# Kernel tuning notes

Hardware: AMD Instinct MI355X
Metric: run time of the kernel (lower is better)

The kernel has to match this reference:

```python
import jax, jax.numpy as jnp
import numpy as np

N_NODES = 50000
N_EDGES = 800000
D_IN = 128
D_OUT = 128


def setup_inputs() -> dict:
    key = jax.random.key(0)
    k1, k2, k3, k4 = jax.random.split(key, 4)
    X = jax.random.normal(k1, (N_NODES, D_IN), dtype=jnp.float32)
    weight = jax.random.normal(k2, (D_IN, D_OUT), dtype=jnp.float32) * (1.0 / np.sqrt(D_OUT))
    edge_src = jax.random.randint(k3, (N_EDGES,), 0, N_NODES, dtype=jnp.int32)
    edge_dst = jax.random.randint(k4, (N_EDGES,), 0, N_NODES, dtype=jnp.int32)
    return {"X": X, "weight": weight, "edge_src": edge_src, "edge_dst": edge_dst}


def reference(X, weight, edge_src, edge_dst):
    # GCN: out = A_hat_hat @ (X @ W), A_hat_hat = D^-1/2 (A + I) D^-1/2
    ones = jnp.ones((edge_src.shape[0],), dtype=X.dtype)
    # node degrees (+1 for implicit self loop, avoids div-by-zero)
    deg = jax.ops.segment_sum(ones, edge_dst, num_segments=N_NODES) + 1.0
    inv_sqrt_deg = jax.lax.rsqrt(deg)  # [N]
    XW = X @ weight  # [N, D_OUT] dense GEMM
    # per-edge normalization 1/sqrt(d_i * d_j)
    norm = inv_sqrt_deg[edge_dst] * inv_sqrt_deg[edge_src]  # [E]
    msg = XW[edge_src] * norm[:, None]  # [E, D_OUT] gather
    agg = jax.ops.segment_sum(msg, edge_dst, num_segments=N_NODES)  # scatter-add
    # self-loop contribution: 1/d_i * XW[i]
    out = agg + XW * (inv_sqrt_deg * inv_sqrt_deg)[:, None]
    return out
```

## Files before the change

### kernel.cpp

```cpp
#include <hip/hip_runtime.h>

#define N_NODES 50000
#define N_EDGES 800000
#define D 128

#define NBLK 256
#define EPB (N_EDGES / NBLK)
#define NBKT 196
#define CAP 6144

typedef __attribute__((ext_vector_type(8))) short bf16x8;
typedef __attribute__((ext_vector_type(4))) float f32x4;

static const size_t OFF_TOT  = 0;
static const size_t OFF_WT   = 1024;
static const size_t OFF_H    = 33792;
static const size_t OFF_BB   = 234496;
static const size_t OFF_DEG  = 435200;
static const size_t OFF_OFFS = 635200;
static const size_t OFF_IVS  = 835200;
static const size_t OFF_REC  = 1235200;
static const size_t OFF_CSR  = 6052096;
static const size_t OFF_XWQ  = 8460544;

#define BM 64
#define NB_GEMM ((N_NODES + BM - 1) / BM)

__device__ __forceinline__ unsigned short f2bf(float f) {
    unsigned int u = __float_as_uint(f);
    unsigned int r = (u + 0x7fffu + ((u >> 16) & 1u)) >> 16;
    return (unsigned short)r;
}
__device__ __forceinline__ float sb(unsigned int u, int i) {
    return (float)((int)(u << (24 - 8 * i)) >> 24);
}

__global__ __launch_bounds__(256) void k_pre(const int* __restrict__ dst,
                                             int* __restrict__ H,
                                             const float* __restrict__ W,
                                             unsigned short* __restrict__ Wt) {
    __shared__ unsigned int cnt[256];
    int bid = blockIdx.x, t = threadIdx.x;
    if (bid >= NBLK) {
        int idx = (bid - NBLK) * 256 + t;
        int n = idx >> 7, k = idx & 127;
        Wt[n * D + k] = f2bf(W[k * D + n]);
        return;
    }
    cnt[t] = 0;
    __syncthreads();
    int e0 = bid * EPB;
    for (int i = t; i < EPB; i += 256)
        atomicAdd(&cnt[dst[e0 + i] >> 8], 1u);
    __syncthreads();
    if (t < NBKT) H[t * NBLK + bid] = (int)cnt[t];
}

__global__ __launch_bounds__(256) void k_pB(const int* __restrict__ H,
                                            int* __restrict__ BB,
                                            int* __restrict__ TOT) {
    int k = blockIdx.x, t = threadIdx.x;
    int w = t >> 6, l = t & 63;
    int v = H[k * NBLK + t];
    int s = v;
    #pragma unroll
    for (int d = 1; d < 64; d <<= 1) {
        int u = __shfl_up(s, d, 64);
        if (l >= d) s += u;
    }
    __shared__ int wtot[4], woff[4];
    if (l == 63) wtot[w] = s;
    __syncthreads();
    if (t == 0) {
        woff[0] = 0; woff[1] = wtot[0];
        woff[2] = wtot[0] + wtot[1]; woff[3] = wtot[0] + wtot[1] + wtot[2];
    }
    __syncthreads();
    int excl = s - v + woff[w];
    BB[k * NBLK + t] = excl;
    if (t == 255) TOT[k] = excl + v;
}

__global__ __launch_bounds__(512) void k_pC(const int* __restrict__ src,
                                            const int* __restrict__ dst,
                                            const int* __restrict__ BB,
                                            unsigned int* __restrict__ rec) {
    __shared__ unsigned int cnt[200];
    __shared__ int myBB[NBKT];
    int b = blockIdx.x, t = threadIdx.x;
    if (t < 200) cnt[t] = 0;
    if (t < NBKT) myBB[t] = t * CAP + BB[t * NBLK + b];
    __syncthreads();
    int e0 = b * EPB;
    for (int i = t; i < EPB; i += 512) {
        int e = e0 + i;
        int d = dst[e];
        int k = d >> 8;
        unsigned int r = atomicAdd(&cnt[k], 1u);
        rec[myBB[k] + (int)r] = (unsigned int)src[e] | ((unsigned int)(d & 255) << 16);
    }
}

__global__ __launch_bounds__(256) void k_mid(const unsigned int* __restrict__ rec,
                                             const int* __restrict__ TOT,
                                             int* __restrict__ deg,
                                             int* __restrict__ offs,
                                             float* __restrict__ ivs,
                                             unsigned short* __restrict__ csr,
                                             const float* __restrict__ X,
                                             const unsigned short* __restrict__ Wt,
                                             char* __restrict__ XWq) {
    __shared__ unsigned short sA[BM * D];
    __shared__ unsigned short sB[D * D];
    __shared__ int wtot[4], woff[4];
    int bid = blockIdx.x;
    int t = threadIdx.x;
    int w = t >> 6, l = t & 63;

    if (bid >= NBKT) {
        int r0 = (bid - NBKT) * BM;

        #pragma unroll
        for (int p = 0; p < 8; ++p) {
            int e = p * 2048 + t * 8;
            int n = e >> 7, k = e & 127;
            uint4 v = *(const uint4*)&Wt[e];
            int idx = n * D + (((k >> 3) ^ (n & 7)) << 3);
            *(uint4*)&sB[idx] = v;
        }
        #pragma unroll
        for (int p = 0; p < 8; ++p) {
            int e = p * 1024 + t * 4;
            int r = e >> 7, c = e & 127;
            int row = r0 + r;
            float4 xv = make_float4(0.f, 0.f, 0.f, 0.f);
            if (row < N_NODES) xv = *(const float4*)&X[row * D + c];
            ushort4 bv;
            bv.x = f2bf(xv.x); bv.y = f2bf(xv.y); bv.z = f2bf(xv.z); bv.w = f2bf(xv.w);
            int idx = r * D + (((c >> 3) ^ (r & 7)) << 3) + (c & 7);
            *(ushort4*)&sA[idx] = bv;
        }
        __syncthreads();

        int arow = w * 16 + (l & 15);
        f32x4 acc[8];
        #pragma unroll
        for (int i = 0; i < 8; ++i) acc[i] = (f32x4){0.f, 0.f, 0.f, 0.f};

        #pragma unroll
        for (int kk = 0; kk < 4; ++kk) {
            int g = kk * 4 + (l >> 4);
            bf16x8 a = *(bf16x8*)&sA[arow * D + ((g ^ (arow & 7)) << 3)];
            #pragma unroll
            for (int nt = 0; nt < 8; ++nt) {
                int nrow = nt * 16 + (l & 15);
                bf16x8 b = *(bf16x8*)&sB[nrow * D + ((g ^ (nrow & 7)) << 3)];
                acc[nt] = __builtin_amdgcn_mfma_f32_16x16x32_bf16(a, b, acc[nt], 0, 0, 0);
            }
        }

        float rmax[4];
        #pragma unroll
        for (int r = 0; r < 4; ++r) {
            float m = 0.f;
            #pragma unroll
            for (int nt = 0; nt < 8; ++nt) m = fmaxf(m, fabsf(acc[nt][r]));
            #pragma unroll
            for (int d = 1; d < 16; d <<= 1) m = fmaxf(m, __shfl_xor(m, d, 64));
            rmax[r] = fmaxf(m, 1e-20f);
        }

        __syncthreads();
        char* sQ = (char*)sA;
        #pragma unroll
        for (int r = 0; r < 4; ++r) {
            float qs = 127.0f / rmax[r];
            int row = w * 16 + (l >> 4) * 4 + r;
            #pragma unroll
            for (int nt = 0; nt < 8; ++nt) {
                float f = acc[nt][r] * qs;
                f = fminf(fmaxf(f, -127.0f), 127.0f);
                sQ[row * D + nt * 16 + (l & 15)] = (char)__float2int_rn(f);
            }
            if ((l & 15) == 0) {
                int m = r0 + row;
                if (m < N_NODES) ivs[m * 2 + 1] = rmax[r] * (1.0f / 127.0f);
            }
        }
        __syncthreads();

        int limit = (N_NODES - r0) * D;
        if (limit > BM * D) limit = BM * D;
        const uint4* q4 = (const uint4*)sQ;
        uint4* dst4 = (uint4*)(XWq + (size_t)r0 * D);
        if (t * 16 < limit) dst4[t] = q4[t];
        if ((t + 256) * 16 < limit) dst4[t + 256] = q4[t + 256];
        return;
    }

    unsigned int* lcnt = (unsigned int*)sA;
    int* off_l = ((int*)sA) + 256;
    int k = bid;
    int base = k * CAP;
    int tot = TOT[k];

    lcnt[t] = 0;
    __syncthreads();
    for (int i = t; i < tot; i += 256)
        atomicAdd(&lcnt[rec[base + i] >> 16], 1u);
    __syncthreads();

    int v = (int)lcnt[t];
    int s = v;
    #pragma unroll
    for (int d = 1; d < 64; d <<= 1) {
        int u = __shfl_up(s, d, 64);
        if (l >= d) s += u;
    }
    if (l == 63) wtot[w] = s;
    __syncthreads();
    if (t == 0) {
        woff[0] = 0; woff[1] = wtot[0];
        woff[2] = wtot[0] + wtot[1]; woff[3] = wtot[0] + wtot[1] + wtot[2];
    }
    __syncthreads();
    int excl = s - v + woff[w];
    off_l[t] = excl;
    int node = k * 256 + t;
    if (node < N_NODES) {
        deg[node] = v;
        ivs[node * 2] = rsqrtf((float)v + 1.0f);
        offs[node] = base + excl;
    }
    __syncthreads();
    lcnt[t] = 0;
    __syncthreads();
    for (int i = t; i < tot; i += 256) {
        unsigned int rc = rec[base + i];
        int dl = rc >> 16;
        unsigned int r = atomicAdd(&lcnt[dl], 1u);
        csr[base + off_l[dl] + (int)r] = (unsigned short)(rc & 0xFFFFu);
    }
}

__global__ __launch_bounds__(256) void k_agg(const char* __restrict__ XWq,
                                             const float2* __restrict__ ivs,
                                             const unsigned short* __restrict__ csr,
                                             const int* __restrict__ offs,
                                             const int* __restrict__ deg,
                                             float* __restrict__ out) {
    int node = blockIdx.x * 4 + (threadIdx.x >> 6);
    if (node >= N_NODES) return;
    int l = threadIdx.x & 63;
    int eg = l >> 4;
    int cl = l & 15;

    int start = offs[node];
    int cnt = deg[node];
    float2 vs0 = ivs[node];
    float invd = vs0.x;

    float acc[8];
    #pragma unroll
    for (int j = 0; j < 8; ++j) acc[j] = 0.f;

    if (eg == 0) {
        float sc = invd * invd * vs0.y;
        uint2 v = *(const uint2*)&XWq[(size_t)node * D + cl * 8];
        acc[0] += sc * sb(v.x, 0); acc[1] += sc * sb(v.x, 1);
        acc[2] += sc * sb(v.x, 2); acc[3] += sc * sb(v.x, 3);
        acc[4] += sc * sb(v.y, 0); acc[5] += sc * sb(v.y, 1);
        acc[6] += sc * sb(v.y, 2); acc[7] += sc * sb(v.y, 3);
    }

    for (int e = eg; e < cnt; e += 16) {
        int s[4];
        #pragma unroll
        for (int u = 0; u < 4; ++u) {
            int ee = e + u * 4;
            s[u] = (ee < cnt) ? (int)csr[start + ee] : -1;
        }
        uint2 v[4];
        float nn[4];
        #pragma unroll
        for (int u = 0; u < 4; ++u) {
            int si = (s[u] >= 0) ? s[u] : s[0];
            v[u] = *(const uint2*)&XWq[(size_t)si * D + cl * 8];
            float2 iv = ivs[si];
            nn[u] = (s[u] >= 0) ? invd * iv.x * iv.y : 0.f;
        }
        #pragma unroll
        for (int u = 0; u < 4; ++u) {
            float n = nn[u];
            acc[0] += n * sb(v[u].x, 0); acc[1] += n * sb(v[u].x, 1);
            acc[2] += n * sb(v[u].x, 2); acc[3] += n * sb(v[u].x, 3);
            acc[4] += n * sb(v[u].y, 0); acc[5] += n * sb(v[u].y, 1);
            acc[6] += n * sb(v[u].y, 2); acc[7] += n * sb(v[u].y, 3);
        }
    }

    #pragma unroll
    for (int j = 0; j < 8; ++j) {
        acc[j] += __shfl_xor(acc[j], 16, 64);
        acc[j] += __shfl_xor(acc[j], 32, 64);
    }

    if (l < 16) {
        float4 v0 = make_float4(acc[0], acc[1], acc[2], acc[3]);
        float4 v1 = make_float4(acc[4], acc[5], acc[6], acc[7]);
        *(float4*)&out[node * D + cl * 8] = v0;
        *(float4*)&out[node * D + cl * 8 + 4] = v1;
    }
}

extern "C" void kernel_launch(void* const* d_in, const int* in_sizes, int n_in,
                              void* d_out, int out_size, void* d_ws, size_t ws_size,
                              hipStream_t stream) {
    const float* X = (const float*)d_in[0];
    const float* W = (const float*)d_in[1];
    const int* esrc = (const int*)d_in[2];
    const int* edst = (const int*)d_in[3];
    float* out = (float*)d_out;

    char* ws = (char*)d_ws;
    int* TOT = (int*)(ws + OFF_TOT);
    unsigned short* Wt = (unsigned short*)(ws + OFF_WT);
    int* H = (int*)(ws + OFF_H);
    int* BB = (int*)(ws + OFF_BB);
    int* deg = (int*)(ws + OFF_DEG);
    int* offs = (int*)(ws + OFF_OFFS);
    float* ivs = (float*)(ws + OFF_IVS);
    unsigned int* rec = (unsigned int*)(ws + OFF_REC);
    unsigned short* csr = (unsigned short*)(ws + OFF_CSR);
    char* XWq = (char*)(ws + OFF_XWQ);

    k_pre<<<NBLK + 64, 256, 0, stream>>>(edst, H, W, Wt);
    k_pB<<<NBKT, 256, 0, stream>>>(H, BB, TOT);
    k_pC<<<NBLK, 512, 0, stream>>>(esrc, edst, BB, rec);
    k_mid<<<NBKT + NB_GEMM, 256, 0, stream>>>(rec, TOT, deg, offs, ivs, csr,
                                              X, Wt, XWq);
    k_agg<<<(N_NODES + 3) / 4, 256, 0, stream>>>(XWq, (const float2*)ivs, csr,
                                                 offs, deg, out);
}
```

Measured before the change: 63.68 us.

## Vectorize edge loads, pad CSR rows, and remap aggregation to 16 lanes per node

Block count for the edge-bucketing passes changes to 250 so each block's edge range is a multiple of four, which lets the histogram and scatter kernels read dst/src as int4. Per-node CSR segments are padded to a multiple of four with zero entries, so aggregation can fetch eight source indices per iteration with two 8-byte loads. The aggregation kernel now gives each node 16 lanes that walk all of its edges with eight gathers in flight, which removes the cross-lane shuffle reduction and packs 16 nodes per block. The trade-off is fewer parallel edge groups per node and reads of a few padded or neighbouring CSR entries whose contributions are masked out.

```diff
diff --git a/kernel.cpp b/kernel.cpp
--- a/kernel.cpp
+++ b/kernel.cpp
@@ -4,8 +4,9 @@
 #define N_EDGES 800000
 #define D 128
 
-#define NBLK 256
+#define NBLK 250
 #define EPB (N_EDGES / NBLK)
+#define NQ (EPB / 4)
 #define NBKT 196
 #define CAP 6144
 
@@ -50,10 +51,15 @@
     cnt[t] = 0;
     __syncthreads();
     int e0 = bid * EPB;
-    for (int i = t; i < EPB; i += 256)
-        atomicAdd(&cnt[dst[e0 + i] >> 8], 1u);
-    __syncthreads();
-    if (t < NBKT) H[t * NBLK + bid] = (int)cnt[t];
+    for (int q = t; q < NQ; q += 256) {
+        int4 d4 = *(const int4*)&dst[e0 + q * 4];
+        atomicAdd(&cnt[d4.x >> 8], 1u);
+        atomicAdd(&cnt[d4.y >> 8], 1u);
+        atomicAdd(&cnt[d4.z >> 8], 1u);
+        atomicAdd(&cnt[d4.w >> 8], 1u);
+    }
+    __syncthreads();
+    if (t < NBKT) H[t * 256 + bid] = (int)cnt[t];
 }
 
 __global__ __launch_bounds__(256) void k_pB(const int* __restrict__ H,
@@ -61,7 +67,7 @@
                                             int* __restrict__ TOT) {
     int k = blockIdx.x, t = threadIdx.x;
     int w = t >> 6, l = t & 63;
-    int v = H[k * NBLK + t];
+    int v = (t < NBLK) ? H[k * 256 + t] : 0;
     int s = v;
     #pragma unroll
     for (int d = 1; d < 64; d <<= 1) {
@@ -77,7 +83,7 @@
     }
     __syncthreads();
     int excl = s - v + woff[w];
-    BB[k * NBLK + t] = excl;
+    BB[k * 256 + t] = excl;
     if (t == 255) TOT[k] = excl + v;
 }
 
@@ -89,15 +95,32 @@
     __shared__ int myBB[NBKT];
     int b = blockIdx.x, t = threadIdx.x;
     if (t < 200) cnt[t] = 0;
-    if (t < NBKT) myBB[t] = t * CAP + BB[t * NBLK + b];
+    if (t < NBKT) myBB[t] = t * CAP + BB[t * 256 + b];
     __syncthreads();
     int e0 = b * EPB;
-    for (int i = t; i < EPB; i += 512) {
-        int e = e0 + i;
-        int d = dst[e];
-        int k = d >> 8;
-        unsigned int r = atomicAdd(&cnt[k], 1u);
-        rec[myBB[k] + (int)r] = (unsigned int)src[e] | ((unsigned int)(d & 255) << 16);
+    for (int q = t; q < NQ; q += 512) {
+        int4 d4 = *(const int4*)&dst[e0 + q * 4];
+        int4 s4 = *(const int4*)&src[e0 + q * 4];
+        {
+            int k = d4.x >> 8;
+            unsigned int r = atomicAdd(&cnt[k], 1u);
+            rec[myBB[k] + (int)r] = (unsigned int)s4.x | ((unsigned int)(d4.x & 255) << 16);
+        }
+        {
+            int k = d4.y >> 8;
+            unsigned int r = atomicAdd(&cnt[k], 1u);
+            rec[myBB[k] + (int)r] = (unsigned int)s4.y | ((unsigned int)(d4.y & 255) << 16);
+        }
+        {
+            int k = d4.z >> 8;
+            unsigned int r = atomicAdd(&cnt[k], 1u);
+            rec[myBB[k] + (int)r] = (unsigned int)s4.z | ((unsigned int)(d4.z & 255) << 16);
+        }
+        {
+            int k = d4.w >> 8;
+            unsigned int r = atomicAdd(&cnt[k], 1u);
+            rec[myBB[k] + (int)r] = (unsigned int)s4.w | ((unsigned int)(d4.w & 255) << 16);
+        }
     }
 }
 
@@ -211,7 +234,8 @@
     __syncthreads();
 
     int v = (int)lcnt[t];
-    int s = v;
+    int vr = (v + 3) & ~3;
+    int s = vr;
     #pragma unroll
     for (int d = 1; d < 64; d <<= 1) {
         int u = __shfl_up(s, d, 64);
@@ -224,7 +248,7 @@
         woff[2] = wtot[0] + wtot[1]; woff[3] = wtot[0] + wtot[1] + wtot[2];
     }
     __syncthreads();
-    int excl = s - v + woff[w];
+    int excl = s - vr + woff[w];
     off_l[t] = excl;
     int node = k * 256 + t;
     if (node < N_NODES) {
@@ -232,6 +256,7 @@
         ivs[node * 2] = rsqrtf((float)v + 1.0f);
         offs[node] = base + excl;
     }
+    for (int j = v; j < vr; ++j) csr[base + excl + j] = 0;
     __syncthreads();
     lcnt[t] = 0;
     __syncthreads();
@@ -249,48 +274,56 @@
                                              const int* __restrict__ offs,
                                              const int* __restrict__ deg,
                                              float* __restrict__ out) {
-    int node = blockIdx.x * 4 + (threadIdx.x >> 6);
-    if (node >= N_NODES) return;
-    int l = threadIdx.x & 63;
-    int eg = l >> 4;
-    int cl = l & 15;
-
-    int start = offs[node];
-    int cnt = deg[node];
-    float2 vs0 = ivs[node];
-    float invd = vs0.x;
+    __shared__ int s_off[16];
+    __shared__ int s_cnt[16];
+    __shared__ float2 s_iv[16];
+    int n0 = blockIdx.x * 16;
+    int t = threadIdx.x;
+    if (t < 16) {
+        int n = n0 + t;
+        int ok = (n < N_NODES);
+        s_off[t] = ok ? offs[n] : 0;
+        s_cnt[t] = ok ? deg[n] : -1;
+        s_iv[t] = ok ? ivs[n] : make_float2(0.f, 0.f);
+    }
+    __syncthreads();
+    int li = t >> 4;
+    int cl = t & 15;
+    int node = n0 + li;
+    int cnt = s_cnt[li];
+    if (cnt < 0) return;
+    int start = s_off[li];
+    float2 vs = s_iv[li];
+    float invd = vs.x;
 
     float acc[8];
-    #pragma unroll
-    for (int j = 0; j < 8; ++j) acc[j] = 0.f;
-
-    if (eg == 0) {
-        float sc = invd * invd * vs0.y;
+    {
+        float sc = invd * invd * vs.y;
         uint2 v = *(const uint2*)&XWq[(size_t)node * D + cl * 8];
-        acc[0] += sc * sb(v.x, 0); acc[1] += sc * sb(v.x, 1);
-        acc[2] += sc * sb(v.x, 2); acc[3] += sc * sb(v.x, 3);
-        acc[4] += sc * sb(v.y, 0); acc[5] += sc * sb(v.y, 1);
-        acc[6] += sc * sb(v.y, 2); acc[7] += sc * sb(v.y, 3);
-    }
-
-    for (int e = eg; e < cnt; e += 16) {
-        int s[4];
-        #pragma unroll
-        for (int u = 0; u < 4; ++u) {
-            int ee = e + u * 4;
-            s[u] = (ee < cnt) ? (int)csr[start + ee] : -1;
-        }
-        uint2 v[4];
-        float nn[4];
-        #pragma unroll
-        for (int u = 0; u < 4; ++u) {
-            int si = (s[u] >= 0) ? s[u] : s[0];
-            v[u] = *(const uint2*)&XWq[(size_t)si * D + cl * 8];
-            float2 iv = ivs[si];
-            nn[u] = (s[u] >= 0) ? invd * iv.x * iv.y : 0.f;
-        }
-        #pragma unroll
-        for (int u = 0; u < 4; ++u) {
+        acc[0] = sc * sb(v.x, 0); acc[1] = sc * sb(v.x, 1);
+        acc[2] = sc * sb(v.x, 2); acc[3] = sc * sb(v.x, 3);
+        acc[4] = sc * sb(v.y, 0); acc[5] = sc * sb(v.y, 1);
+        acc[6] = sc * sb(v.y, 2); acc[7] = sc * sb(v.y, 3);
+    }
+
+    for (int e = 0; e < cnt; e += 8) {
+        uint2 ca = *(const uint2*)&csr[start + e];
+        uint2 cb = *(const uint2*)&csr[start + e + 4];
+        int si[8];
+        si[0] = ca.x & 0xffff; si[1] = ca.x >> 16;
+        si[2] = ca.y & 0xffff; si[3] = ca.y >> 16;
+        si[4] = cb.x & 0xffff; si[5] = cb.x >> 16;
+        si[6] = cb.y & 0xffff; si[7] = cb.y >> 16;
+        uint2 v[8];
+        float nn[8];
+        #pragma unroll
+        for (int u = 0; u < 8; ++u) {
+            v[u] = *(const uint2*)&XWq[(size_t)si[u] * D + cl * 8];
+            float2 iv = ivs[si[u]];
+            nn[u] = (e + u < cnt) ? invd * iv.x * iv.y : 0.f;
+        }
+        #pragma unroll
+        for (int u = 0; u < 8; ++u) {
             float n = nn[u];
             acc[0] += n * sb(v[u].x, 0); acc[1] += n * sb(v[u].x, 1);
             acc[2] += n * sb(v[u].x, 2); acc[3] += n * sb(v[u].x, 3);
@@ -299,18 +332,10 @@
         }
     }
 
-    #pragma unroll
-    for (int j = 0; j < 8; ++j) {
-        acc[j] += __shfl_xor(acc[j], 16, 64);
-        acc[j] += __shfl_xor(acc[j], 32, 64);
-    }
-
-    if (l < 16) {
-        float4 v0 = make_float4(acc[0], acc[1], acc[2], acc[3]);
-        float4 v1 = make_float4(acc[4], acc[5], acc[6], acc[7]);
-        *(float4*)&out[node * D + cl * 8] = v0;
-        *(float4*)&out[node * D + cl * 8 + 4] = v1;
-    }
+    float4 o0 = make_float4(acc[0], acc[1], acc[2], acc[3]);
+    float4 o1 = make_float4(acc[4], acc[5], acc[6], acc[7]);
+    *(float4*)&out[node * D + cl * 8] = o0;
+    *(float4*)&out[node * D + cl * 8 + 4] = o1;
 }
 
 extern "C" void kernel_launch(void* const* d_in, const int* in_sizes, int n_in,
@@ -339,6 +364,6 @@
     k_pC<<<NBLK, 512, 0, stream>>>(esrc, edst, BB, rec);
     k_mid<<<NBKT + NB_GEMM, 256, 0, stream>>>(rec, TOT, deg, offs, ivs, csr,
                                               X, Wt, XWq);
-    k_agg<<<(N_NODES + 3) / 4, 256, 0, stream>>>(XWq, (const float2*)ivs, csr,
-                                                 offs, deg, out);
-}
+    k_agg<<<(N_NODES + 15) / 16, 256, 0, stream>>>(XWq, (const float2*)ivs, csr,
+                                                   offs, deg, out);
+}
```

Result: faster. 62.27 us (-2.2%).
